# Optimization experiments

Measured on AMD Instinct MI355X. Metric: run time of the kernel, lower is better.

The kernel has to match this reference:

```python
import jax, jax.numpy as jnp
import numpy as np

B, Q, C, P, A = 32, 300, 81, 300, 29


def box_cxcywh_to_xyxy(b):
    cx, cy, w, h = b[..., 0], b[..., 1], b[..., 2], b[..., 3]
    return jnp.stack([cx - 0.5 * w, cy - 0.5 * h, cx + 0.5 * w, cy + 0.5 * h], axis=-1)


def setup_inputs() -> dict:
    key = jax.random.key(0)
    k1, k2, k3, k4, k5 = jax.random.split(key, 5)
    pred_logits = jax.random.normal(k1, (B, Q, C), dtype=jnp.float32)
    pred_boxes = jax.random.uniform(k2, (B, Q, 4), dtype=jnp.float32)
    pred_actions = jax.random.normal(k3, (B, P, A), dtype=jnp.float32)
    pred_rel_pairs = jax.random.randint(k4, (B, P, 2), 0, Q, dtype=jnp.int64)
    # realistic image sizes (h, w) in pixels
    target_sizes = 480.0 + 320.0 * jax.random.uniform(k5, (B, 2), dtype=jnp.float32)
    return {
        'pred_logits': pred_logits,
        'pred_boxes': pred_boxes,
        'pred_actions': pred_actions,
        'pred_rel_pairs': pred_rel_pairs,
        'target_sizes': target_sizes,
    }


def reference(pred_logits, pred_boxes, pred_actions, pred_rel_pairs, target_sizes):
    threshold = 0.0
    # class scores/labels (last class is no-object, excluded from max)
    prob = jax.nn.softmax(pred_logits, axis=-1)
    scores = prob[..., :-1].max(-1)          # [B,Q]
    labels = prob[..., :-1].argmax(-1)       # [B,Q]
    # boxes to xyxy, scaled to image size
    boxes = box_cxcywh_to_xyxy(pred_boxes)   # [B,Q,4]
    img_h, img_w = target_sizes[:, 0], target_sizes[:, 1]
    scale_fct = jnp.stack([img_w, img_h, img_w, img_h], axis=1)  # [B,4]
    boxes = boxes * scale_fct[:, None, :]
    # vcoco path: pairwise action score matrix via one fused scatter
    pair_actions = jax.nn.sigmoid(pred_actions)          # [B,P,A]
    h_idx = pred_rel_pairs[:, :, 0]                      # [B,P]
    o_idx = pred_rel_pairs[:, :, 1]                      # [B,P]
    # original: if h_idx == o_idx -> o_idx = -1 (i.e. last column K of K+1)
    o_idx = jnp.where(h_idx == o_idx, Q, o_idx)
    b_idx = jnp.arange(B, dtype=h_idx.dtype)[:, None]    # [B,1] -> broadcast [B,P]
    score = jnp.zeros((B, Q, Q + 1, A), dtype=pair_actions.dtype)
    score = score.at[b_idx, h_idx, o_idx].set(pair_actions)
    score = jnp.transpose(score, (0, 3, 1, 2))           # [B,A,Q,Q+1]
    # ragged boolean masks (returned as masks instead of data-dependent slices)
    h_mask = (labels == 1) & (scores > threshold)        # human rows
    o_mask = jnp.concatenate([scores > threshold,
                              jnp.ones((B, 1), dtype=bool)], axis=1)  # K+1 cols
    return scores, labels, boxes, score, h_mask, o_mask
```

## Files before the change

kernel.cpp:

```cpp
#include <hip/hip_runtime.h>
#include <hip/hip_bf16.h>

#define BB 32
#define QQ 300
#define CC 81
#define PP 300
#define AA 29

constexpr long long OFF_SCORES = 0;
constexpr long long OFF_LABELS = OFF_SCORES + (long long)BB * QQ;
constexpr long long OFF_BOXES  = OFF_LABELS + (long long)BB * QQ;
constexpr long long OFF_SCORE  = OFF_BOXES  + (long long)BB * QQ * 4;
constexpr long long SCORE_ELEMS = (long long)BB * AA * QQ * (QQ + 1);
constexpr long long OFF_HMASK  = OFF_SCORE + SCORE_ELEMS;
constexpr long long OFF_OMASK  = OFF_HMASK + (long long)BB * QQ;

constexpr int SLOTS = QQ * (QQ + 1);
constexpr int SCT_THREADS = 512;


__global__ void cls_box_mask_kernel(const float* __restrict__ logits,
                                    const float* __restrict__ boxes_in,
                                    const float* __restrict__ tsize,
                                    float* __restrict__ out) {
    int t = blockIdx.x * blockDim.x + threadIdx.x;
    if (t >= BB * QQ) return;
    int b = t / QQ;
    int q = t - b * QQ;

    const float* l = logits + (long long)t * CC;

    float m = -1e30f;
    float best = -1e30f;
    int am = 0;
    for (int c = 0; c < CC; ++c) {
        float x = l[c];
        m = fmaxf(m, x);
        if (c < CC - 1 && x > best) { best = x; am = c; }
    }
    float s = 0.0f;
    for (int c = 0; c < CC; ++c) {
        s += __expf(l[c] - m);
    }
    float score = __expf(best - m) / s;

    out[OFF_SCORES + t] = score;
    out[OFF_LABELS + t] = (float)am;

    float cx = boxes_in[4 * (long long)t + 0];
    float cy = boxes_in[4 * (long long)t + 1];
    float w  = boxes_in[4 * (long long)t + 2];
    float h  = boxes_in[4 * (long long)t + 3];
    float img_h = tsize[2 * b + 0];
    float img_w = tsize[2 * b + 1];
    out[OFF_BOXES + 4 * (long long)t + 0] = (cx - 0.5f * w) * img_w;
    out[OFF_BOXES + 4 * (long long)t + 1] = (cy - 0.5f * h) * img_h;
    out[OFF_BOXES + 4 * (long long)t + 2] = (cx + 0.5f * w) * img_w;
    out[OFF_BOXES + 4 * (long long)t + 3] = (cy + 0.5f * h) * img_h;

    out[OFF_HMASK + t] = (am == 1 && score > 0.0f) ? 1.0f : 0.0f;
    out[OFF_OMASK + (long long)b * (QQ + 1) + q] = (score > 0.0f) ? 1.0f : 0.0f;
    if (q == 0) out[OFF_OMASK + (long long)b * (QQ + 1) + QQ] = 1.0f;
}

__global__ void scatter_kernel(const int* __restrict__ pairs,
                               const float* __restrict__ actions,
                               float* __restrict__ out) {
    __shared__ int s_key[PP];
    __shared__ int s_win[PP];
    __shared__ int nz;
    int tid = threadIdx.x;
    int b = blockIdx.x;
    if (tid == 0) nz = 0;
    __syncthreads();

    int local = 0;
    for (int i = tid; i < BB * PP; i += blockDim.x) local |= pairs[2 * i + 1];
    if (local) atomicOr(&nz, 1);
    __syncthreads();
    bool is64 = (nz == 0);

    if (tid < PP) {
        int h, o;
        if (is64) {
            h = pairs[((long long)(b * PP + tid)) * 4 + 0];
            o = pairs[((long long)(b * PP + tid)) * 4 + 2];
        } else {
            h = pairs[((long long)(b * PP + tid)) * 2 + 0];
            o = pairs[((long long)(b * PP + tid)) * 2 + 1];
        }
        if (h == o) o = QQ;
        s_key[tid] = h * (QQ + 1) + o;
    }
    __syncthreads();

    if (tid < PP) {
        int k = s_key[tid];
        int win = 1;
        for (int p2 = tid + 1; p2 < PP; ++p2) {
            if (s_key[p2] == k) { win = 0; break; }
        }
        s_win[tid] = win;
    }
    __syncthreads();

    const float* actb = actions + (long long)b * PP * AA;
    float* scoreb = out + OFF_SCORE + (long long)b * AA * SLOTS;
    for (int i = tid; i < PP * AA; i += SCT_THREADS) {
        int p = i / AA;
        int a = i - p * AA;
        if (!s_win[p]) continue;
        float x = actb[p * AA + a];
        float sg = 1.0f / (1.0f + __expf(-x));
        scoreb[(long long)a * SLOTS + s_key[p]] = sg;
    }
}

extern "C" void kernel_launch(void* const* d_in, const int* in_sizes, int n_in,
                              void* d_out, int out_size, void* d_ws, size_t ws_size,
                              hipStream_t stream) {
    const float* logits   = (const float*)d_in[0];
    const float* boxes_in = (const float*)d_in[1];
    const float* actions  = (const float*)d_in[2];
    const int*   pairs    = (const int*)d_in[3];
    const float* tsize    = (const float*)d_in[4];
    float* out = (float*)d_out;

    hipMemsetAsync((char*)d_out + OFF_SCORE * sizeof(float), 0,
                   (size_t)SCORE_ELEMS * sizeof(float), stream);

    int n = BB * QQ;
    cls_box_mask_kernel<<<(n + 255) / 256, 256, 0, stream>>>(logits, boxes_in, tsize, out);
    scatter_kernel<<<BB, SCT_THREADS, 0, stream>>>(pairs, actions, out);
}
```

Before: 412.2 us.

## Fuse zero-fill, classification and scatter into one kernel with counter sync

Replaces the memset plus two kernel launches with a single kernel. Most blocks zero the large score tensor using vectorized stores, while 32 blocks compute the classification, box and mask outputs and prepare scatter keys in parallel. The scatter blocks then spin on a global atomic counter until all fill blocks finish, which removes the launch gaps and overlaps the small work with the fill. This relies on the fill blocks being scheduled while the scatter blocks spin, which holds here because 2048 blocks of 256 threads fit on the device, and it needs a workspace for the counter.

Result: slower. 724.6 us (+75.8%).

```diff
diff --git a/kernel.cpp b/kernel.cpp
--- a/kernel.cpp
+++ b/kernel.cpp
@@ -16,8 +16,125 @@
 constexpr long long OFF_OMASK  = OFF_HMASK + (long long)BB * QQ;
 
 constexpr int SLOTS = QQ * (QQ + 1);
-constexpr int SCT_THREADS = 512;
-
+constexpr int N4 = (int)(SCORE_ELEMS / 4);
+constexpr int NBLK = 2048;
+constexpr int SCT_BLOCKS = BB;
+constexpr int FILL_BLOCKS = NBLK - SCT_BLOCKS;
+
+typedef float f32x4 __attribute__((ext_vector_type(4)));
+
+
+__global__ __launch_bounds__(256) void fused_kernel(const float* __restrict__ logits,
+                                                    const float* __restrict__ boxes_in,
+                                                    const float* __restrict__ tsize,
+                                                    const int* __restrict__ pairs,
+                                                    const float* __restrict__ actions,
+                                                    float* __restrict__ out,
+                                                    int* __restrict__ ctr) {
+    const int bid = blockIdx.x;
+    const int tid = threadIdx.x;
+
+    if (bid >= SCT_BLOCKS) {
+        f32x4* p = (f32x4*)(out + OFF_SCORE);
+        f32x4 z = (f32x4)0.0f;
+        for (int i = (bid - SCT_BLOCKS) * 256 + tid; i < N4; i += FILL_BLOCKS * 256) {
+            p[i] = z;
+        }
+        __threadfence();
+        __syncthreads();
+        if (tid == 0) {
+            __hip_atomic_fetch_add(ctr, 1, __ATOMIC_RELEASE, __HIP_MEMORY_SCOPE_AGENT);
+        }
+        return;
+    }
+
+    const int b = bid;
+
+    for (int q = tid; q < QQ; q += 256) {
+        int t = b * QQ + q;
+        const float* l = logits + (long long)t * CC;
+        float m = -1e30f, best = -1e30f;
+        int am = 0;
+        for (int c = 0; c < CC; ++c) {
+            float x = l[c];
+            m = fmaxf(m, x);
+            if (c < CC - 1 && x > best) { best = x; am = c; }
+        }
+        float s = 0.0f;
+        for (int c = 0; c < CC; ++c) s += __expf(l[c] - m);
+        float score = __expf(best - m) / s;
+
+        out[OFF_SCORES + t] = score;
+        out[OFF_LABELS + t] = (float)am;
+
+        float cx = boxes_in[4 * (long long)t + 0];
+        float cy = boxes_in[4 * (long long)t + 1];
+        float w  = boxes_in[4 * (long long)t + 2];
+        float h  = boxes_in[4 * (long long)t + 3];
+        float img_h = tsize[2 * b + 0];
+        float img_w = tsize[2 * b + 1];
+        out[OFF_BOXES + 4 * (long long)t + 0] = (cx - 0.5f * w) * img_w;
+        out[OFF_BOXES + 4 * (long long)t + 1] = (cy - 0.5f * h) * img_h;
+        out[OFF_BOXES + 4 * (long long)t + 2] = (cx + 0.5f * w) * img_w;
+        out[OFF_BOXES + 4 * (long long)t + 3] = (cy + 0.5f * h) * img_h;
+
+        out[OFF_HMASK + t] = (am == 1 && score > 0.0f) ? 1.0f : 0.0f;
+        out[OFF_OMASK + (long long)b * (QQ + 1) + q] = (score > 0.0f) ? 1.0f : 0.0f;
+        if (q == 0) out[OFF_OMASK + (long long)b * (QQ + 1) + QQ] = 1.0f;
+    }
+
+    __shared__ int s_key[PP];
+    __shared__ int s_win[PP];
+    __shared__ int nz;
+    if (tid == 0) nz = 0;
+    __syncthreads();
+    int local = 0;
+    for (int i = tid; i < BB * PP; i += 256) local |= pairs[2 * i + 1];
+    if (local) atomicOr(&nz, 1);
+    __syncthreads();
+    bool is64 = (nz == 0);
+
+    for (int pp = tid; pp < PP; pp += 256) {
+        int h, o;
+        if (is64) {
+            h = pairs[((long long)(b * PP + pp)) * 4 + 0];
+            o = pairs[((long long)(b * PP + pp)) * 4 + 2];
+        } else {
+            h = pairs[((long long)(b * PP + pp)) * 2 + 0];
+            o = pairs[((long long)(b * PP + pp)) * 2 + 1];
+        }
+        if (h == o) o = QQ;
+        s_key[pp] = h * (QQ + 1) + o;
+    }
+    __syncthreads();
+    for (int pp = tid; pp < PP; pp += 256) {
+        int k = s_key[pp];
+        int win = 1;
+        for (int p2 = pp + 1; p2 < PP; ++p2) {
+            if (s_key[p2] == k) { win = 0; break; }
+        }
+        s_win[pp] = win;
+    }
+    __syncthreads();
+
+    if (tid == 0) {
+        while (__hip_atomic_load(ctr, __ATOMIC_ACQUIRE, __HIP_MEMORY_SCOPE_AGENT) < FILL_BLOCKS) {
+            __builtin_amdgcn_s_sleep(8);
+        }
+    }
+    __syncthreads();
+
+    const float* actb = actions + (long long)b * PP * AA;
+    float* scoreb = out + OFF_SCORE + (long long)b * AA * SLOTS;
+    for (int i = tid; i < PP * AA; i += 256) {
+        int p = i / AA;
+        int a = i - p * AA;
+        if (!s_win[p]) continue;
+        float x = actb[i];
+        float sg = 1.0f / (1.0f + __expf(-x));
+        scoreb[(long long)a * SLOTS + s_key[p]] = sg;
+    }
+}
 
 __global__ void cls_box_mask_kernel(const float* __restrict__ logits,
                                     const float* __restrict__ boxes_in,
@@ -27,11 +144,8 @@
     if (t >= BB * QQ) return;
     int b = t / QQ;
     int q = t - b * QQ;
-
     const float* l = logits + (long long)t * CC;
-
-    float m = -1e30f;
-    float best = -1e30f;
+    float m = -1e30f, best = -1e30f;
     int am = 0;
     for (int c = 0; c < CC; ++c) {
         float x = l[c];
@@ -39,14 +153,10 @@
         if (c < CC - 1 && x > best) { best = x; am = c; }
     }
     float s = 0.0f;
-    for (int c = 0; c < CC; ++c) {
-        s += __expf(l[c] - m);
-    }
+    for (int c = 0; c < CC; ++c) s += __expf(l[c] - m);
     float score = __expf(best - m) / s;
-
     out[OFF_SCORES + t] = score;
     out[OFF_LABELS + t] = (float)am;
-
     float cx = boxes_in[4 * (long long)t + 0];
     float cy = boxes_in[4 * (long long)t + 1];
     float w  = boxes_in[4 * (long long)t + 2];
@@ -57,7 +167,6 @@
     out[OFF_BOXES + 4 * (long long)t + 1] = (cy - 0.5f * h) * img_h;
     out[OFF_BOXES + 4 * (long long)t + 2] = (cx + 0.5f * w) * img_w;
     out[OFF_BOXES + 4 * (long long)t + 3] = (cy + 0.5f * h) * img_h;
-
     out[OFF_HMASK + t] = (am == 1 && score > 0.0f) ? 1.0f : 0.0f;
     out[OFF_OMASK + (long long)b * (QQ + 1) + q] = (score > 0.0f) ? 1.0f : 0.0f;
     if (q == 0) out[OFF_OMASK + (long long)b * (QQ + 1) + QQ] = 1.0f;
@@ -73,13 +182,11 @@
     int b = blockIdx.x;
     if (tid == 0) nz = 0;
     __syncthreads();
-
     int local = 0;
     for (int i = tid; i < BB * PP; i += blockDim.x) local |= pairs[2 * i + 1];
     if (local) atomicOr(&nz, 1);
     __syncthreads();
     bool is64 = (nz == 0);
-
     if (tid < PP) {
         int h, o;
         if (is64) {
@@ -93,7 +200,6 @@
         s_key[tid] = h * (QQ + 1) + o;
     }
     __syncthreads();
-
     if (tid < PP) {
         int k = s_key[tid];
         int win = 1;
@@ -103,14 +209,13 @@
         s_win[tid] = win;
     }
     __syncthreads();
-
     const float* actb = actions + (long long)b * PP * AA;
     float* scoreb = out + OFF_SCORE + (long long)b * AA * SLOTS;
-    for (int i = tid; i < PP * AA; i += SCT_THREADS) {
+    for (int i = tid; i < PP * AA; i += 512) {
         int p = i / AA;
         int a = i - p * AA;
         if (!s_win[p]) continue;
-        float x = actb[p * AA + a];
+        float x = actb[i];
         float sg = 1.0f / (1.0f + __expf(-x));
         scoreb[(long long)a * SLOTS + s_key[p]] = sg;
     }
@@ -126,10 +231,16 @@
     const float* tsize    = (const float*)d_in[4];
     float* out = (float*)d_out;
 
-    hipMemsetAsync((char*)d_out + OFF_SCORE * sizeof(float), 0,
-                   (size_t)SCORE_ELEMS * sizeof(float), stream);
-
-    int n = BB * QQ;
-    cls_box_mask_kernel<<<(n + 255) / 256, 256, 0, stream>>>(logits, boxes_in, tsize, out);
-    scatter_kernel<<<BB, SCT_THREADS, 0, stream>>>(pairs, actions, out);
-}
+    if (d_ws != nullptr && ws_size >= sizeof(int)) {
+        int* ctr = (int*)d_ws;
+        hipMemsetAsync(ctr, 0, sizeof(int), stream);
+        fused_kernel<<<NBLK, 256, 0, stream>>>(logits, boxes_in, tsize, pairs,
+                                               actions, out, ctr);
+    } else {
+        hipMemsetAsync((char*)d_out + OFF_SCORE * sizeof(float), 0,
+                       (size_t)SCORE_ELEMS * sizeof(float), stream);
+        int n = BB * QQ;
+        cls_box_mask_kernel<<<(n + 255) / 256, 256, 0, stream>>>(logits, boxes_in, tsize, out);
+        scatter_kernel<<<BB, 512, 0, stream>>>(pairs, actions, out);
+    }
+}
```
